# Kernel optimization log

Measured on AMD Instinct MI355X. Metric: run time of the kernel, lower is better.

## Reference

```python
import jax, jax.numpy as jnp
import numpy as np

T, D, E, K = 8192, 7168, 256, 8
G, LG = 8, 4  # n_expert_groups, n_limited_groups
ROUTE_SCALE = 2.5


def setup_inputs() -> dict:
    key = jax.random.key(0)
    k1, k2, k3 = jax.random.split(key, 3)
    x = jax.random.normal(k1, (T, D), dtype=jnp.float32)
    W = jax.random.normal(k2, (E, D), dtype=jnp.float32) * (1.0 / np.sqrt(D))
    bias = jax.random.normal(k3, (E,), dtype=jnp.float32) * 0.01
    return {"x": x, "W": W, "bias": bias}


def reference(x, W, bias):
    # linear scorer: [T, E]
    logits = jnp.einsum("td,ed->te", x, W)
    original_scores = jax.nn.sigmoid(logits)
    scores = original_scores + bias  # bias only affects routing, not weights

    # group selection: reshape [T, G, E//G]; group score = sum of top-2 (bias path)
    scores_g = scores.reshape(T, G, E // G)
    group_scores = jax.lax.top_k(scores_g, 2)[0].sum(axis=-1)  # [T, G]
    _, gidx = jax.lax.top_k(group_scores, LG)  # [T, LG]
    keep = jnp.any(jnp.arange(G)[None, None, :] == gidx[:, :, None], axis=1)  # [T, G]
    scores_masked = jnp.where(keep[:, :, None], scores_g, -jnp.inf).reshape(T, E)

    # final top-k experts
    _, indices = jax.lax.top_k(scores_masked, K)  # [T, K] int32
    weights = jnp.take_along_axis(original_scores, indices, axis=1)  # [T, K]
    weights = weights / weights.sum(axis=-1, keepdims=True)  # sigmoid normalization
    weights = weights * ROUTE_SCALE
    weights = weights.astype(x.dtype)

    # per-expert token counts (indices unique per row, so scatter(1)+sum == histogram)
    counts = jnp.zeros((E,), dtype=jnp.int32).at[indices.reshape(-1)].add(1)
    return weights, indices.astype(jnp.int64), counts
```

## Files before the change

### kernel.cpp

```cpp
#include <hip/hip_runtime.h>
#include <math.h>
#include <stdint.h>

#define T_TOK 8192
#define D_DIM 7168
#define E_EXP 256
#define K_SEL 8
#define G_GRP 8
#define LG_GRP 4
#define ROUTE_SCALE 2.5f

#define BM 128
#define BN 128
#define BK 64
#define NKT (D_DIM / BK)
#define KT_HALF (NKT / 2)
#define SCALE_LO 2048.0f
#define INV_SCALE (1.0f / 2048.0f)

typedef _Float16 half_t;
typedef _Float16 half8 __attribute__((ext_vector_type(8)));
typedef float f32x4 __attribute__((ext_vector_type(4)));

#define WF_HALVES_PER_H (2 * 112 * 16 * 512)

__device__ __forceinline__ void load_lds16(const void* g, void* l) {
    __builtin_amdgcn_global_load_lds(
        (const __attribute__((address_space(1))) uint32_t*)g,
        (__attribute__((address_space(3))) uint32_t*)l, 16, 0, 0);
}

__global__ __launch_bounds__(256)
void convert_W_kernel(const float* __restrict__ W, half_t* __restrict__ Wf) {
    const int u = blockIdx.x * 256 + threadIdx.x;
    const int slot = u & 63;
    const int ks   = (u >> 6) & 1;
    const int p    = (u >> 7) & 7;
    const int t2   = u >> 10;
    const int kt   = t2 % 112;
    const int nb   = t2 / 112;
    const int e = nb * 128 + p * 16 + (slot & 15);
    const int k = kt * 64 + ks * 32 + (slot >> 4) * 8;

    const float* src = W + (size_t)e * D_DIM + k;
    float4 v0 = *(const float4*)src;
    float4 v1 = *(const float4*)(src + 4);
    float f[8] = {v0.x, v0.y, v0.z, v0.w, v1.x, v1.y, v1.z, v1.w};
    half8 hi, lo;
    #pragma unroll
    for (int j = 0; j < 8; j++) {
        const half_t h = (half_t)f[j];
        hi[j] = h;
        lo[j] = (half_t)((f[j] - (float)h) * SCALE_LO);
    }
    *(half8*)&Wf[(size_t)u * 8] = hi;
    *(half8*)&Wf[(size_t)WF_HALVES_PER_H + (size_t)u * 8] = lo;
}

__global__ __launch_bounds__(256, 1)
void gemm_logits_f16split(const float* __restrict__ x,
                          const half_t* __restrict__ Wf,
                          float* __restrict__ plane0,
                          float* __restrict__ plane1) {
    __shared__ __align__(16) half_t Ah[8 * 2 * 64 * 8];
    __shared__ __align__(16) half_t Al[8 * 2 * 64 * 8];
    __shared__ __align__(16) half_t Bbuf[2][32][512];

    const int tid = threadIdx.x;
    const int bid = blockIdx.x;
    const int g     = bid & 7;
    const int j     = bid >> 3;
    const int nb    = g & 1;
    const int split = (g >> 1) & 1;
    const int m_blk = ((g >> 2) << 5) + j;
    const int row0 = m_blk * BM;
    const int ks0  = split * KT_HALF;

    const float* __restrict__ xA = x + (size_t)row0 * D_DIM;
    float* __restrict__ plane = split ? plane1 : plane0;

    const int wave = tid >> 6, lane = tid & 63;
    const int q = lane >> 4;
    const int mp0 = (wave >> 1) * 4;
    const int np0 = (wave & 1) * 4;

    float4 pa[4][2];
    half8 hreg[4], lreg[4];

    auto load_A = [&](int kt) {
        const int kbase = kt * BK;
        #pragma unroll
        for (int i = 0; i < 4; i++) {
            const int u = i * 256 + tid;
            const int r = u >> 3, k8 = u & 7;
            const float* p = xA + (size_t)r * D_DIM + kbase + k8 * 8;
            pa[i][0] = *(const float4*)p;
            pa[i][1] = *(const float4*)(p + 4);
        }
    };

    auto convert_A = [&]() {
        #pragma unroll
        for (int i = 0; i < 4; i++) {
            float f[8] = {pa[i][0].x, pa[i][0].y, pa[i][0].z, pa[i][0].w,
                          pa[i][1].x, pa[i][1].y, pa[i][1].z, pa[i][1].w};
            #pragma unroll
            for (int jj = 0; jj < 8; jj++) {
                const half_t h = (half_t)f[jj];
                hreg[i][jj] = h;
                lreg[i][jj] = (half_t)((f[jj] - (float)h) * SCALE_LO);
            }
        }
    };

    auto write_A = [&]() {
        #pragma unroll
        for (int i = 0; i < 4; i++) {
            const int u = i * 256 + tid;
            const int r = u >> 3, k8 = u & 7;
            const int m = r & 15, qq = k8 & 3, kss = k8 >> 2;
            const int slot = (m + 16 * qq) ^ k8;
            const int off = (((r >> 4) * 2 + kss) * 64 + slot) * 8;
            *(half8*)&Ah[off] = hreg[i];
            *(half8*)&Al[off] = lreg[i];
        }
    };

    auto issue_B = [&](int tt) {
        const int kt = ks0 + tt;
        half_t* bb = &Bbuf[tt & 1][0][0];
        #pragma unroll
        for (int i = 0; i < 8; i++) {
            const int s32 = i * 4 + wave;
            const int h = s32 >> 4, sl = s32 & 15;
            const half_t* src = Wf +
                ((size_t)((h * 2 + nb) * 112 + kt) * 16 + sl) * 512 + lane * 8;
            load_lds16(src, bb + s32 * 512);
        }
    };

    f32x4 ach[4][4] = {}, acc[4][4] = {};

    auto compute = [&](int tt) {
        const half_t* bb = &Bbuf[tt & 1][0][0];
        #pragma unroll
        for (int ks = 0; ks < 2; ks++) {
            const int slot = lane ^ ((ks << 2) | q);
            half8 ah[4], al[4], bh[4], bl[4];
            #pragma unroll
            for (int mi = 0; mi < 4; mi++) {
                const int off = (((mp0 + mi) * 2 + ks) * 64 + slot) * 8;
                ah[mi] = *(const half8*)&Ah[off];
                al[mi] = *(const half8*)&Al[off];
            }
            #pragma unroll
            for (int ni = 0; ni < 4; ni++) {
                const int s32 = (np0 + ni) * 2 + ks;
                bh[ni] = *(const half8*)&bb[s32 * 512 + lane * 8];
                bl[ni] = *(const half8*)&bb[(16 + s32) * 512 + lane * 8];
            }
            #pragma unroll
            for (int mi = 0; mi < 4; mi++)
                #pragma unroll
                for (int ni = 0; ni < 4; ni++) {
                    ach[mi][ni] = __builtin_amdgcn_mfma_f32_16x16x32_f16(ah[mi], bh[ni], ach[mi][ni], 0, 0, 0);
                    acc[mi][ni] = __builtin_amdgcn_mfma_f32_16x16x32_f16(ah[mi], bl[ni], acc[mi][ni], 0, 0, 0);
                    acc[mi][ni] = __builtin_amdgcn_mfma_f32_16x16x32_f16(al[mi], bh[ni], acc[mi][ni], 0, 0, 0);
                }
        }
    };

    issue_B(0);
    load_A(ks0);

    #pragma unroll 1
    for (int tt = 0; tt < KT_HALF; tt++) {
        convert_A();
        __syncthreads();
        write_A();
        __syncthreads();
        if (tt + 1 < KT_HALF) {
            issue_B(tt + 1);
            load_A(ks0 + tt + 1);
        }
        compute(tt);
    }

    const int col0 = nb * BN;
    #pragma unroll
    for (int mi = 0; mi < 4; mi++)
        #pragma unroll
        for (int ni = 0; ni < 4; ni++) {
            const f32x4 vh = ach[mi][ni];
            const f32x4 vc = acc[mi][ni];
            const int ex = col0 + (np0 + ni) * 16 + (lane & 15);
            #pragma unroll
            for (int r = 0; r < 4; r++) {
                const int tok = row0 + (mp0 + mi) * 16 + q * 4 + r;
                plane[(size_t)tok * E_EXP + ex] = vh[r] + vc[r] * INV_SCALE;
            }
        }
}

__global__ __launch_bounds__(256)
void routing_kernel(const float* __restrict__ plane0,
                    const float* __restrict__ plane1,
                    const float* __restrict__ bias,
                    float* __restrict__ out_w,
                    float* __restrict__ out_i) {
    const int wave = threadIdx.x >> 6;
    const int lane = threadIdx.x & 63;
    const int t    = blockIdx.x * 4 + wave;

    const float4 l0 = *(const float4*)(plane0 + (size_t)t * E_EXP + lane * 4);
    const float4 l1 = *(const float4*)(plane1 + (size_t)t * E_EXP + lane * 4);
    const float4 bi = *(const float4*)(bias + lane * 4);
    float lg[4] = {l0.x + l1.x, l0.y + l1.y, l0.z + l1.z, l0.w + l1.w};

    float orig[4], s[4];
    #pragma unroll
    for (int j = 0; j < 4; j++)
        orig[j] = 1.0f / (1.0f + expf(-lg[j]));
    s[0] = orig[0] + bi.x; s[1] = orig[1] + bi.y;
    s[2] = orig[2] + bi.z; s[3] = orig[3] + bi.w;

    float p1 = fmaxf(s[0], s[1]), p2 = fminf(s[0], s[1]);
    float q1 = fmaxf(s[2], s[3]), q2 = fminf(s[2], s[3]);
    float m1 = fmaxf(p1, q1);
    float m2 = fmaxf(fminf(p1, q1), (p1 >= q1) ? p2 : q2);

    #pragma unroll
    for (int off = 1; off <= 4; off <<= 1) {
        float o1 = __shfl_xor(m1, off);
        float o2 = __shfl_xor(m2, off);
        float M1 = fmaxf(m1, o1);
        float M2 = fmaxf(fminf(m1, o1), (m1 >= o1) ? m2 : o2);
        m1 = M1; m2 = M2;
    }
    const float gscore = m1 + m2;

    const int g = lane >> 3;
    int cnt = 0;
    #pragma unroll
    for (int j = 0; j < G_GRP; j++) {
        float gj = __shfl(gscore, j * 8);
        cnt += (gj > gscore || (gj == gscore && j < g)) ? 1 : 0;
    }
    const bool keep = (cnt < LG_GRP);

    float smask[4];
    #pragma unroll
    for (int j = 0; j < 4; j++) smask[j] = keep ? s[j] : -INFINITY;

    float wsum = 0.0f, my_o = 0.0f;
    int my_i = 0;

    #pragma unroll
    for (int k = 0; k < K_SEL; k++) {
        float bv = smask[0]; float bo = orig[0]; int bs = 0;
        if (smask[1] > bv) { bv = smask[1]; bo = orig[1]; bs = 1; }
        if (smask[2] > bv) { bv = smask[2]; bo = orig[2]; bs = 2; }
        if (smask[3] > bv) { bv = smask[3]; bo = orig[3]; bs = 3; }
        int bidx = lane * 4 + bs;

        #pragma unroll
        for (int off = 32; off >= 1; off >>= 1) {
            float ov = __shfl_xor(bv, off);
            float oo = __shfl_xor(bo, off);
            int   oi = __shfl_xor(bidx, off);
            if (ov > bv || (ov == bv && oi < bidx)) { bv = ov; bo = oo; bidx = oi; }
        }
        wsum += bo;
        if (lane == k) { my_o = bo; my_i = bidx; }
        if ((bidx >> 2) == lane) {
            const int sl = bidx & 3;
            smask[0] = (sl == 0) ? -INFINITY : smask[0];
            smask[1] = (sl == 1) ? -INFINITY : smask[1];
            smask[2] = (sl == 2) ? -INFINITY : smask[2];
            smask[3] = (sl == 3) ? -INFINITY : smask[3];
        }
    }

    if (lane < K_SEL) {
        out_w[(size_t)t * K_SEL + lane] = my_o * ROUTE_SCALE / wsum;
        out_i[(size_t)t * K_SEL + lane] = (float)my_i;
    }
}

__global__ __launch_bounds__(256)
void count_kernel(const float* __restrict__ idxf, float* __restrict__ out_c) {
    const float fe = (float)blockIdx.x;
    int c = 0;
    const float4* p = (const float4*)idxf;
    for (int i = threadIdx.x; i < (T_TOK * K_SEL / 4); i += 256) {
        float4 v = p[i];
        c += (v.x == fe) + (v.y == fe) + (v.z == fe) + (v.w == fe);
    }
    __shared__ int red[4];
    #pragma unroll
    for (int off = 32; off >= 1; off >>= 1) c += __shfl_down(c, off);
    if ((threadIdx.x & 63) == 0) red[threadIdx.x >> 6] = c;
    __syncthreads();
    if (threadIdx.x == 0)
        out_c[blockIdx.x] = (float)(red[0] + red[1] + red[2] + red[3]);
}

extern "C" void kernel_launch(void* const* d_in, const int* in_sizes, int n_in,
                              void* d_out, int out_size, void* d_ws, size_t ws_size,
                              hipStream_t stream) {
    const float* x    = (const float*)d_in[0];
    const float* W    = (const float*)d_in[1];
    const float* bias = (const float*)d_in[2];

    float* out   = (float*)d_out;
    float* out_w = out;
    float* out_i = out + (size_t)T_TOK * K_SEL;
    float* out_c = out + (size_t)2 * T_TOK * K_SEL;

    float* plane0 = (float*)d_ws;
    float* plane1 = plane0 + (size_t)T_TOK * E_EXP;
    half_t* Wf    = (half_t*)(plane1 + (size_t)T_TOK * E_EXP);

    hipLaunchKernelGGL(convert_W_kernel, dim3(896), dim3(256), 0, stream, W, Wf);
    hipLaunchKernelGGL(gemm_logits_f16split, dim3(256), dim3(256), 0, stream,
                       x, Wf, plane0, plane1);
    hipLaunchKernelGGL(routing_kernel, dim3(T_TOK / 4), dim3(256), 0, stream,
                       plane0, plane1, bias, out_w, out_i);
    hipLaunchKernelGGL(count_kernel, dim3(E_EXP), dim3(256), 0, stream,
                       out_i, out_c);
}
```

Measured before the change: 435.8 us.

## Split-K into four parts, single-buffer B, and allow two blocks per CU

Raises the K-split from two to four, doubling the GEMM grid to 512 blocks, and sets launch bounds to allow two resident blocks per CU. To fit, the B tile in LDS goes from double to single buffering, and the pipeline is reordered so the B load is issued alongside the A write and the A convert overlaps after compute. The aim is to fill the GPU better and hide latency through occupancy rather than in-block double buffering. The cost is an extra partial-sum plane to write and read in routing, tighter register limits, and loss of the explicit B prefetch overlap.

```diff
diff --git a/kernel.cpp b/kernel.cpp
--- a/kernel.cpp
+++ b/kernel.cpp
@@ -14,7 +14,6 @@
 #define BN 128
 #define BK 64
 #define NKT (D_DIM / BK)
-#define KT_HALF (NKT / 2)
 #define SCALE_LO 2048.0f
 #define INV_SCALE (1.0f / 2048.0f)
 
@@ -57,27 +56,26 @@
     *(half8*)&Wf[(size_t)WF_HALVES_PER_H + (size_t)u * 8] = lo;
 }
 
-__global__ __launch_bounds__(256, 1)
+__global__ __launch_bounds__(256, 2)
 void gemm_logits_f16split(const float* __restrict__ x,
                           const half_t* __restrict__ Wf,
-                          float* __restrict__ plane0,
-                          float* __restrict__ plane1) {
+                          float* __restrict__ planes,
+                          int kt_len, int gshift) {
     __shared__ __align__(16) half_t Ah[8 * 2 * 64 * 8];
     __shared__ __align__(16) half_t Al[8 * 2 * 64 * 8];
-    __shared__ __align__(16) half_t Bbuf[2][32][512];
+    __shared__ __align__(16) half_t Bbuf[32][512];
 
     const int tid = threadIdx.x;
     const int bid = blockIdx.x;
-    const int g     = bid & 7;
-    const int j     = bid >> 3;
+    const int g     = bid & ((1 << gshift) - 1);
+    const int j     = bid >> gshift;
     const int nb    = g & 1;
-    const int split = (g >> 1) & 1;
-    const int m_blk = ((g >> 2) << 5) + j;
-    const int row0 = m_blk * BM;
-    const int ks0  = split * KT_HALF;
+    const int split = g >> 1;
+    const int row0 = j * BM;
+    const int ks0  = split * kt_len;
 
     const float* __restrict__ xA = x + (size_t)row0 * D_DIM;
-    float* __restrict__ plane = split ? plane1 : plane0;
+    float* __restrict__ plane = planes + (size_t)split * T_TOK * E_EXP;
 
     const int wave = tid >> 6, lane = tid & 63;
     const int q = lane >> 4;
@@ -128,7 +126,7 @@
 
     auto issue_B = [&](int tt) {
         const int kt = ks0 + tt;
-        half_t* bb = &Bbuf[tt & 1][0][0];
+        half_t* bb = &Bbuf[0][0];
         #pragma unroll
         for (int i = 0; i < 8; i++) {
             const int s32 = i * 4 + wave;
@@ -141,8 +139,8 @@
 
     f32x4 ach[4][4] = {}, acc[4][4] = {};
 
-    auto compute = [&](int tt) {
-        const half_t* bb = &Bbuf[tt & 1][0][0];
+    auto compute = [&]() {
+        const half_t* bb = &Bbuf[0][0];
         #pragma unroll
         for (int ks = 0; ks < 2; ks++) {
             const int slot = lane ^ ((ks << 2) | q);
@@ -170,20 +168,18 @@
         }
     };
 
-    issue_B(0);
     load_A(ks0);
+    convert_A();
 
     #pragma unroll 1
-    for (int tt = 0; tt < KT_HALF; tt++) {
-        convert_A();
+    for (int tt = 0; tt < kt_len; tt++) {
         __syncthreads();
         write_A();
+        issue_B(tt);
         __syncthreads();
-        if (tt + 1 < KT_HALF) {
-            issue_B(tt + 1);
-            load_A(ks0 + tt + 1);
-        }
-        compute(tt);
+        if (tt + 1 < kt_len) load_A(ks0 + tt + 1);
+        compute();
+        if (tt + 1 < kt_len) convert_A();
     }
 
     const int col0 = nb * BN;
@@ -203,19 +199,22 @@
 }
 
 __global__ __launch_bounds__(256)
-void routing_kernel(const float* __restrict__ plane0,
-                    const float* __restrict__ plane1,
+void routing_kernel(const float* __restrict__ planes,
                     const float* __restrict__ bias,
                     float* __restrict__ out_w,
-                    float* __restrict__ out_i) {
+                    float* __restrict__ out_i,
+                    int nsplit) {
     const int wave = threadIdx.x >> 6;
     const int lane = threadIdx.x & 63;
     const int t    = blockIdx.x * 4 + wave;
 
-    const float4 l0 = *(const float4*)(plane0 + (size_t)t * E_EXP + lane * 4);
-    const float4 l1 = *(const float4*)(plane1 + (size_t)t * E_EXP + lane * 4);
+    float lg[4] = {0.f, 0.f, 0.f, 0.f};
+    for (int s = 0; s < nsplit; s++) {
+        const float4 l = *(const float4*)(planes + (size_t)s * T_TOK * E_EXP +
+                                          (size_t)t * E_EXP + lane * 4);
+        lg[0] += l.x; lg[1] += l.y; lg[2] += l.z; lg[3] += l.w;
+    }
     const float4 bi = *(const float4*)(bias + lane * 4);
-    float lg[4] = {l0.x + l1.x, l0.y + l1.y, l0.z + l1.z, l0.w + l1.w};
 
     float orig[4], s[4];
     #pragma unroll
@@ -317,15 +316,24 @@
     float* out_i = out + (size_t)T_TOK * K_SEL;
     float* out_c = out + (size_t)2 * T_TOK * K_SEL;
 
-    float* plane0 = (float*)d_ws;
-    float* plane1 = plane0 + (size_t)T_TOK * E_EXP;
-    half_t* Wf    = (half_t*)(plane1 + (size_t)T_TOK * E_EXP);
+    const size_t planeN  = (size_t)T_TOK * E_EXP;
+    const size_t wfBytes = (size_t)2 * WF_HALVES_PER_H * sizeof(half_t);
+
+    int nsplit = 4;
+    if (ws_size != 0 && ws_size < 4 * planeN * sizeof(float) + wfBytes)
+        nsplit = 2;
+    const int gshift = (nsplit == 4) ? 3 : 2;
+    const int kt_len = NKT / nsplit;
+    const int grid   = 64 * 2 * nsplit;
+
+    float* planes = (float*)d_ws;
+    half_t* Wf    = (half_t*)(planes + (size_t)nsplit * planeN);
 
     hipLaunchKernelGGL(convert_W_kernel, dim3(896), dim3(256), 0, stream, W, Wf);
-    hipLaunchKernelGGL(gemm_logits_f16split, dim3(256), dim3(256), 0, stream,
-                       x, Wf, plane0, plane1);
+    hipLaunchKernelGGL(gemm_logits_f16split, dim3(grid), dim3(256), 0, stream,
+                       x, Wf, planes, kt_len, gshift);
     hipLaunchKernelGGL(routing_kernel, dim3(T_TOK / 4), dim3(256), 0, stream,
-                       plane0, plane1, bias, out_w, out_i);
+                       planes, bias, out_w, out_i, nsplit);
     hipLaunchKernelGGL(count_kernel, dim3(E_EXP), dim3(256), 0, stream,
                        out_i, out_c);
 }
```

Result: slower. 519.0 us (+19.1%).
